# Kernel optimization log

Measured on AMD Instinct MI355X. Metric: run time of the kernel, lower is better.

Reference implementation:

```python
import jax, jax.numpy as jnp
import numpy as np

# irreps_in = irreps_out = 256x0e + 128x1o + 64x2e
MULS = [256, 128, 64]      # multiplicities per irrep
IRDIMS = [1, 3, 5]          # 2l+1 for l=0,1,2
N = 200000                  # number of atoms / nodes
DIM = sum(m * d for m, d in zip(MULS, IRDIMS))          # 960
WNUM = sum(m * m for m in MULS)                          # 86016
BNUM = MULS[0]                                           # bias only on scalar (0e) outputs


def setup_inputs() -> dict:
    key = jax.random.key(0)
    k1, k2, k3 = jax.random.split(key, 3)
    x = jax.random.normal(k1, (N, DIM), dtype=jnp.float32)
    w = jax.random.normal(k2, (WNUM,), dtype=jnp.float32)
    b = jax.random.normal(k3, (BNUM,), dtype=jnp.float32) * 0.1
    return {"x": x, "w": w, "b": b}


def reference(x, w, b):
    # Faithful to _codegen_linear with f_in=f_out=None, shared_weights=True:
    # per-irrep block einsum 'uw,zui->zwi' scaled by 1/sqrt(mul_in), plus bias on 0e block.
    n = x.shape[0]
    outs = []
    xoff = 0
    woff = 0
    for mul, d in zip(MULS, IRDIMS):
        blk = x[:, xoff:xoff + mul * d].reshape(n, mul, d)          # (N, u, i)
        W = w[woff:woff + mul * mul].reshape(mul, mul)              # (u, w)
        pw = mul ** -0.5                                            # path_weight (element norm)
        o = pw * jnp.einsum('uw,nui->nwi', W, blk)                  # (N, w, i)
        o = o.reshape(n, mul * d)
        if d == 1:  # scalar irrep: bias path, path_weight = 1
            o = o + b.reshape(1, mul)
        outs.append(o)
        xoff += mul * d
        woff += mul * mul
    return jnp.concatenate(outs, axis=-1)  # (N, 960)
```

## Files before the change

### kernel.cpp

```cpp
#include <hip/hip_runtime.h>


typedef short frag8 __attribute__((ext_vector_type(8)));
typedef float f32x4 __attribute__((ext_vector_type(4)));
typedef unsigned int u32;
typedef u32 u32x4 __attribute__((ext_vector_type(4)));

#define ST0 1040
#define ST1 1552
#define ST2 1296

static __device__ __forceinline__ short f2bf(float f) {
    union { float f; unsigned u; } v; v.f = f;
    unsigned r = (v.u + 0x7FFFu + ((v.u >> 16) & 1u)) >> 16;
    return (short)r;
}

static __device__ __forceinline__ u32 cvtpk(float lo, float hi) {
    u32 r;
    asm("v_cvt_pk_bf16_f32 %0, %1, %2" : "=v"(r) : "v"(lo), "v"(hi));
    return r;
}

static __device__ __forceinline__ frag8 asfrag(u32x4 u) {
    union { u32x4 u; frag8 f; } t; t.u = u; return t.f;
}

#define MFMA(a, b, c) __builtin_amdgcn_mfma_f32_16x16x32_bf16((a), (b), (c), 0, 0, 0)

__global__ __launch_bounds__(256) void prep_kernel(const float* __restrict__ w,
                                                   short* __restrict__ wf) {
    int e = blockIdx.x * 256 + threadIdx.x;
    int f = e >> 9;
    int r = e & 511;
    int l = r >> 3, j = r & 7;
    int l15 = l & 15, lg = l >> 4;
    int kk = 4 * lg + (j & 3) + 16 * (j >> 2);
    int u, wc, woff, mul; float scale;
    if (f < 128) {
        int nt = f >> 3, s = f & 7;
        u = 32 * s + kk; wc = nt * 16 + l15; woff = 0;     mul = 256; scale = 0.0625f;
    } else if (f < 160) {
        int g = f - 128, nt = g >> 2, s = g & 3;
        u = 32 * s + kk; wc = nt * 16 + l15; woff = 65536; mul = 128; scale = 0.088388347648318447f;
    } else {
        int g = f - 160, nt = g >> 1, s = g & 1;
        u = 32 * s + kk; wc = nt * 16 + l15; woff = 81920; mul = 64;  scale = 0.125f;
    }
    wf[e] = f2bf(scale * w[woff + u * mul + wc]);
}

static __device__ __forceinline__ void gload_lds16(const void* g, void* l) {
    __builtin_amdgcn_global_load_lds(
        (const __attribute__((address_space(1))) unsigned int*)g,
        (__attribute__((address_space(3))) unsigned int*)l, 16, 0, 0);
}

__global__ __launch_bounds__(256) void lin_t32(const float* __restrict__ x,
                                               const short* __restrict__ wf,
                                               const float* __restrict__ bias,
                                               float* __restrict__ out) {
    __shared__ __align__(16) char smem[32 * ST1];
    const int tid = threadIdx.x, lane = tid & 63, wv = tid >> 6;
    const int l15 = lane & 15, lg = lane >> 4;
    const int fam = blockIdx.y;
    const long rowbase = (long)blockIdx.x * 32;
    const char* __restrict__ xb = (const char*)x + rowbase * 3840;
    char* __restrict__ ob = (char*)out + rowbase * 3840;
    const frag8* __restrict__ wfr = (const frag8*)wf;

    if (fam == 0) {
        f32x4 bv[4];
        #pragma unroll
        for (int q = 0; q < 4; ++q)
            bv[q] = *(const f32x4*)(bias + (4 * wv + q) * 16 + 4 * lg);
        #pragma unroll
        for (int r8 = 0; r8 < 8; ++r8) {
            int r = 8 * wv + r8;
            gload_lds16(xb + (long)r * 3840 + (long)lane * 16, smem + r * ST0);
        }
        __syncthreads();

        const char* sbA = smem + l15 * ST0;
        frag8 a0[8];
        #pragma unroll
        for (int s = 0; s < 8; ++s) {
            const f32x4 v0 = *(const f32x4*)(sbA + (8 * s + lg) * 16);
            const f32x4 v1 = *(const f32x4*)(sbA + (8 * s + 4 + lg) * 16);
            u32x4 t = { cvtpk(v0[0], v0[1]), cvtpk(v0[2], v0[3]),
                        cvtpk(v1[0], v1[1]), cvtpk(v1[2], v1[3]) };
            a0[s] = asfrag(t);
        }
        __syncthreads();

        #pragma unroll
        for (int q = 0; q < 4; ++q) {
            const int nt = 4 * wv + q;
            f32x4 acc = {0.f, 0.f, 0.f, 0.f};
            #pragma unroll
            for (int s = 0; s < 8; ++s)
                acc = MFMA(wfr[(nt * 8 + s) * 64 + lane], a0[s], acc);
            const int g0 = nt * 4 + lg;
            *(f32x4*)(smem + l15 * ST0 + g0 * 16) = acc + bv[q];
        }
        const char* sbB = smem + (16 + l15) * ST0;
        frag8 a0b[8];
        #pragma unroll
        for (int s = 0; s < 8; ++s) {
            const f32x4 v0 = *(const f32x4*)(sbB + (8 * s + lg) * 16);
            const f32x4 v1 = *(const f32x4*)(sbB + (8 * s + 4 + lg) * 16);
            u32x4 t = { cvtpk(v0[0], v0[1]), cvtpk(v0[2], v0[3]),
                        cvtpk(v1[0], v1[1]), cvtpk(v1[2], v1[3]) };
            a0b[s] = asfrag(t);
        }
        __syncthreads();

        #pragma unroll
        for (int q = 0; q < 4; ++q) {
            const int nt = 4 * wv + q;
            f32x4 acc = {0.f, 0.f, 0.f, 0.f};
            #pragma unroll
            for (int s = 0; s < 8; ++s)
                acc = MFMA(wfr[(nt * 8 + s) * 64 + lane], a0b[s], acc);
            const int g0 = nt * 4 + lg;
            *(f32x4*)(smem + (16 + l15) * ST0 + g0 * 16) = acc + bv[q];
        }
        __syncthreads();

        #pragma unroll
        for (int j = 0; j < 8; ++j) {
            int c = j * 256 + tid, r = c >> 6, g = c & 63;
            f32x4 v = *(const f32x4*)(smem + r * ST0 + g * 16);
            *(f32x4*)(ob + (long)r * 3840 + g * 16) = v;
        }
    } else if (fam == 1) {
        frag8 w1[8];
        #pragma unroll
        for (int q = 0; q < 2; ++q)
            #pragma unroll
            for (int s = 0; s < 4; ++s)
                w1[q * 4 + s] = wfr[(128 + (2 * wv + q) * 4 + s) * 64 + lane];

        #pragma unroll
        for (int r8 = 0; r8 < 8; ++r8) {
            int r = 8 * wv + r8;
            gload_lds16(xb + (long)r * 3840 + 1024 + (long)lane * 16, smem + r * ST1);
            if (lane < 32)
                gload_lds16(xb + (long)r * 3840 + 2048 + (long)lane * 16,
                            smem + r * ST1 + 1024);
        }
        __syncthreads();

        {
            const char* sb = smem + l15 * ST1;
            u32x4 a1u[12];
            #pragma unroll
            for (int s = 0; s < 4; ++s) {
                #pragma unroll
                for (int h = 0; h < 2; ++h) {
                    const int cb = 24 * s + 12 * h + 3 * lg;
                    const f32x4 q0 = *(const f32x4*)(sb + (cb    ) * 16);
                    const f32x4 q1 = *(const f32x4*)(sb + (cb + 1) * 16);
                    const f32x4 q2 = *(const f32x4*)(sb + (cb + 2) * 16);
                    a1u[0 + s][2 * h]     = cvtpk(q0[0], q0[3]);
                    a1u[0 + s][2 * h + 1] = cvtpk(q1[2], q2[1]);
                    a1u[4 + s][2 * h]     = cvtpk(q0[1], q1[0]);
                    a1u[4 + s][2 * h + 1] = cvtpk(q1[3], q2[2]);
                    a1u[8 + s][2 * h]     = cvtpk(q0[2], q1[1]);
                    a1u[8 + s][2 * h + 1] = cvtpk(q2[0], q2[3]);
                }
            }
            __syncthreads();
            #pragma unroll
            for (int q = 0; q < 2; ++q) {
                const int nt = 2 * wv + q;
                f32x4 c0 = {0.f,0.f,0.f,0.f}, c1 = {0.f,0.f,0.f,0.f}, c2 = {0.f,0.f,0.f,0.f};
                #pragma unroll
                for (int s = 0; s < 4; ++s) {
                    frag8 bw = w1[q * 4 + s];
                    c0 = MFMA(bw, asfrag(a1u[0 + s]), c0);
                    c1 = MFMA(bw, asfrag(a1u[4 + s]), c1);
                    c2 = MFMA(bw, asfrag(a1u[8 + s]), c2);
                }
                const int g0 = 3 * (nt * 4 + lg);
                char* wb = smem + l15 * ST1;
                *(f32x4*)(wb + (g0    ) * 16) = (f32x4){c0[0], c1[0], c2[0], c0[1]};
                *(f32x4*)(wb + (g0 + 1) * 16) = (f32x4){c1[1], c2[1], c0[2], c1[2]};
                *(f32x4*)(wb + (g0 + 2) * 16) = (f32x4){c2[2], c0[3], c1[3], c2[3]};
            }
        }
        {
            const char* sb = smem + (16 + l15) * ST1;
            u32x4 a1u[12];
            #pragma unroll
            for (int s = 0; s < 4; ++s) {
                #pragma unroll
                for (int h = 0; h < 2; ++h) {
                    const int cb = 24 * s + 12 * h + 3 * lg;
                    const f32x4 q0 = *(const f32x4*)(sb + (cb    ) * 16);
                    const f32x4 q1 = *(const f32x4*)(sb + (cb + 1) * 16);
                    const f32x4 q2 = *(const f32x4*)(sb + (cb + 2) * 16);
                    a1u[0 + s][2 * h]     = cvtpk(q0[0], q0[3]);
                    a1u[0 + s][2 * h + 1] = cvtpk(q1[2], q2[1]);
                    a1u[4 + s][2 * h]     = cvtpk(q0[1], q1[0]);
                    a1u[4 + s][2 * h + 1] = cvtpk(q1[3], q2[2]);
                    a1u[8 + s][2 * h]     = cvtpk(q0[2], q1[1]);
                    a1u[8 + s][2 * h + 1] = cvtpk(q2[0], q2[3]);
                }
            }
            __syncthreads();
            #pragma unroll
            for (int q = 0; q < 2; ++q) {
                const int nt = 2 * wv + q;
                f32x4 c0 = {0.f,0.f,0.f,0.f}, c1 = {0.f,0.f,0.f,0.f}, c2 = {0.f,0.f,0.f,0.f};
                #pragma unroll
                for (int s = 0; s < 4; ++s) {
                    frag8 bw = w1[q * 4 + s];
                    c0 = MFMA(bw, asfrag(a1u[0 + s]), c0);
                    c1 = MFMA(bw, asfrag(a1u[4 + s]), c1);
                    c2 = MFMA(bw, asfrag(a1u[8 + s]), c2);
                }
                const int g0 = 3 * (nt * 4 + lg);
                char* wb = smem + (16 + l15) * ST1;
                *(f32x4*)(wb + (g0    ) * 16) = (f32x4){c0[0], c1[0], c2[0], c0[1]};
                *(f32x4*)(wb + (g0 + 1) * 16) = (f32x4){c1[1], c2[1], c0[2], c1[2]};
                *(f32x4*)(wb + (g0 + 2) * 16) = (f32x4){c2[2], c0[3], c1[3], c2[3]};
            }
        }
        __syncthreads();
        #pragma unroll
        for (int j = 0; j < 12; ++j) {
            int c = j * 256 + tid, r = c / 96, g = c - r * 96;
            f32x4 v = *(const f32x4*)(smem + r * ST1 + g * 16);
            *(f32x4*)(ob + (long)r * 3840 + 1024 + g * 16) = v;
        }
    } else {
        frag8 w2[2];
        #pragma unroll
        for (int s = 0; s < 2; ++s)
            w2[s] = wfr[(160 + wv * 2 + s) * 64 + lane];

        #pragma unroll
        for (int r8 = 0; r8 < 8; ++r8) {
            int r = 8 * wv + r8;
            gload_lds16(xb + (long)r * 3840 + 2560 + (long)lane * 16, smem + r * ST2);
            if (lane < 16)
                gload_lds16(xb + (long)r * 3840 + 3584 + (long)lane * 16,
                            smem + r * ST2 + 1024);
        }
        __syncthreads();

        #pragma unroll
        for (int half = 0; half < 2; ++half) {
            const int rbase = 16 * half;
            const char* sb = smem + (rbase + l15) * ST2;
            u32x4 a2u[10];
            #pragma unroll
            for (int s = 0; s < 2; ++s) {
                #pragma unroll
                for (int h = 0; h < 2; ++h) {
                    const int cb = 40 * s + 20 * h + 5 * lg;
                    const f32x4 q0 = *(const f32x4*)(sb + (cb    ) * 16);
                    const f32x4 q1 = *(const f32x4*)(sb + (cb + 1) * 16);
                    const f32x4 q2 = *(const f32x4*)(sb + (cb + 2) * 16);
                    const f32x4 q3 = *(const f32x4*)(sb + (cb + 3) * 16);
                    const f32x4 q4 = *(const f32x4*)(sb + (cb + 4) * 16);
                    a2u[0 + s][2 * h]     = cvtpk(q0[0], q1[1]);
                    a2u[0 + s][2 * h + 1] = cvtpk(q2[2], q3[3]);
                    a2u[2 + s][2 * h]     = cvtpk(q0[1], q1[2]);
                    a2u[2 + s][2 * h + 1] = cvtpk(q2[3], q4[0]);
                    a2u[4 + s][2 * h]     = cvtpk(q0[2], q1[3]);
                    a2u[4 + s][2 * h + 1] = cvtpk(q3[0], q4[1]);
                    a2u[6 + s][2 * h]     = cvtpk(q0[3], q2[0]);
                    a2u[6 + s][2 * h + 1] = cvtpk(q3[1], q4[2]);
                    a2u[8 + s][2 * h]     = cvtpk(q1[0], q2[1]);
                    a2u[8 + s][2 * h + 1] = cvtpk(q3[2], q4[3]);
                }
            }
            __syncthreads();
            {
                f32x4 c0 = {0.f,0.f,0.f,0.f}, c1 = {0.f,0.f,0.f,0.f}, c2 = {0.f,0.f,0.f,0.f},
                      c3 = {0.f,0.f,0.f,0.f}, c4 = {0.f,0.f,0.f,0.f};
                #pragma unroll
                for (int s = 0; s < 2; ++s) {
                    frag8 bw = w2[s];
                    c0 = MFMA(bw, asfrag(a2u[0 + s]), c0);
                    c1 = MFMA(bw, asfrag(a2u[2 + s]), c1);
                    c2 = MFMA(bw, asfrag(a2u[4 + s]), c2);
                    c3 = MFMA(bw, asfrag(a2u[6 + s]), c3);
                    c4 = MFMA(bw, asfrag(a2u[8 + s]), c4);
                }
                const int g0 = 5 * (wv * 4 + lg);
                char* wb = smem + (rbase + l15) * ST2;
                *(f32x4*)(wb + (g0    ) * 16) = (f32x4){c0[0], c1[0], c2[0], c3[0]};
                *(f32x4*)(wb + (g0 + 1) * 16) = (f32x4){c4[0], c0[1], c1[1], c2[1]};
                *(f32x4*)(wb + (g0 + 2) * 16) = (f32x4){c3[1], c4[1], c0[2], c1[2]};
                *(f32x4*)(wb + (g0 + 3) * 16) = (f32x4){c2[2], c3[2], c4[2], c0[3]};
                *(f32x4*)(wb + (g0 + 4) * 16) = (f32x4){c1[3], c2[3], c3[3], c4[3]};
            }
        }
        __syncthreads();
        #pragma unroll
        for (int j = 0; j < 10; ++j) {
            int c = j * 256 + tid, r = c / 80, g = c - r * 80;
            f32x4 v = *(const f32x4*)(smem + r * ST2 + g * 16);
            *(f32x4*)(ob + (long)r * 3840 + 2560 + g * 16) = v;
        }
    }
}

extern "C" void kernel_launch(void* const* d_in, const int* in_sizes, int n_in,
                              void* d_out, int out_size, void* d_ws, size_t ws_size,
                              hipStream_t stream) {
    const float* x = (const float*)d_in[0];
    const float* w = (const float*)d_in[1];
    const float* b = (const float*)d_in[2];
    float* out = (float*)d_out;
    short* wf  = (short*)d_ws;

    hipLaunchKernelGGL(prep_kernel, dim3(336), dim3(256), 0, stream, w, wf);
    hipLaunchKernelGGL(lin_t32, dim3(6250, 3), dim3(256), 0, stream,
                       x, wf, b, out);
}
```

Measured before the change: 324.4 us.

## Split fused per-irrep kernel into three specialized launches and merge half-tile phases

Replaces the single kernel, which branched on blockIdx.y to pick the irrep family, with three separate kernels. Each kernel sizes its shared memory to its own family, so the l=0 and l=2 kernels can fit more blocks per CU. Within each kernel, both 16-row halves are converted to bf16 before a single barrier, which removes intermediate syncthreads and lets their MFMAs interleave. The cost is more register pressure from holding both halves' fragments, plus two extra launches that run back to back instead of concurrently.

```diff
diff --git a/kernel.cpp b/kernel.cpp
--- a/kernel.cpp
+++ b/kernel.cpp
@@ -56,256 +56,241 @@
         (__attribute__((address_space(3))) unsigned int*)l, 16, 0, 0);
 }
 
-__global__ __launch_bounds__(256) void lin_t32(const float* __restrict__ x,
-                                               const short* __restrict__ wf,
-                                               const float* __restrict__ bias,
-                                               float* __restrict__ out) {
-    __shared__ __align__(16) char smem[32 * ST1];
+__global__ __launch_bounds__(256) void lin_a0(const float* __restrict__ x,
+                                              const short* __restrict__ wf,
+                                              const float* __restrict__ bias,
+                                              float* __restrict__ out) {
+    __shared__ __align__(16) char smem[32 * ST0];
     const int tid = threadIdx.x, lane = tid & 63, wv = tid >> 6;
     const int l15 = lane & 15, lg = lane >> 4;
-    const int fam = blockIdx.y;
     const long rowbase = (long)blockIdx.x * 32;
     const char* __restrict__ xb = (const char*)x + rowbase * 3840;
     char* __restrict__ ob = (char*)out + rowbase * 3840;
     const frag8* __restrict__ wfr = (const frag8*)wf;
 
-    if (fam == 0) {
-        f32x4 bv[4];
-        #pragma unroll
-        for (int q = 0; q < 4; ++q)
-            bv[q] = *(const f32x4*)(bias + (4 * wv + q) * 16 + 4 * lg);
-        #pragma unroll
-        for (int r8 = 0; r8 < 8; ++r8) {
-            int r = 8 * wv + r8;
-            gload_lds16(xb + (long)r * 3840 + (long)lane * 16, smem + r * ST0);
-        }
-        __syncthreads();
-
-        const char* sbA = smem + l15 * ST0;
-        frag8 a0[8];
+    f32x4 bv[4];
+    #pragma unroll
+    for (int q = 0; q < 4; ++q)
+        bv[q] = *(const f32x4*)(bias + (4 * wv + q) * 16 + 4 * lg);
+
+    #pragma unroll
+    for (int r8 = 0; r8 < 8; ++r8) {
+        int r = 8 * wv + r8;
+        gload_lds16(xb + (long)r * 3840 + (long)lane * 16, smem + r * ST0);
+    }
+    __syncthreads();
+
+    const char* sbA = smem + l15 * ST0;
+    const char* sbB = smem + (16 + l15) * ST0;
+    frag8 a0[8], a0b[8];
+    #pragma unroll
+    for (int s = 0; s < 8; ++s) {
+        const f32x4 v0 = *(const f32x4*)(sbA + (8 * s + lg) * 16);
+        const f32x4 v1 = *(const f32x4*)(sbA + (8 * s + 4 + lg) * 16);
+        u32x4 t = { cvtpk(v0[0], v0[1]), cvtpk(v0[2], v0[3]),
+                    cvtpk(v1[0], v1[1]), cvtpk(v1[2], v1[3]) };
+        a0[s] = asfrag(t);
+        const f32x4 w0 = *(const f32x4*)(sbB + (8 * s + lg) * 16);
+        const f32x4 w1v = *(const f32x4*)(sbB + (8 * s + 4 + lg) * 16);
+        u32x4 t2 = { cvtpk(w0[0], w0[1]), cvtpk(w0[2], w0[3]),
+                     cvtpk(w1v[0], w1v[1]), cvtpk(w1v[2], w1v[3]) };
+        a0b[s] = asfrag(t2);
+    }
+    __syncthreads();
+
+    #pragma unroll
+    for (int q = 0; q < 4; ++q) {
+        const int nt = 4 * wv + q;
+        f32x4 accA = {0.f, 0.f, 0.f, 0.f};
+        f32x4 accB = {0.f, 0.f, 0.f, 0.f};
         #pragma unroll
         for (int s = 0; s < 8; ++s) {
-            const f32x4 v0 = *(const f32x4*)(sbA + (8 * s + lg) * 16);
-            const f32x4 v1 = *(const f32x4*)(sbA + (8 * s + 4 + lg) * 16);
-            u32x4 t = { cvtpk(v0[0], v0[1]), cvtpk(v0[2], v0[3]),
-                        cvtpk(v1[0], v1[1]), cvtpk(v1[2], v1[3]) };
-            a0[s] = asfrag(t);
-        }
-        __syncthreads();
-
-        #pragma unroll
-        for (int q = 0; q < 4; ++q) {
-            const int nt = 4 * wv + q;
-            f32x4 acc = {0.f, 0.f, 0.f, 0.f};
+            frag8 bw = wfr[(nt * 8 + s) * 64 + lane];
+            accA = MFMA(bw, a0[s], accA);
+            accB = MFMA(bw, a0b[s], accB);
+        }
+        const int g0 = nt * 4 + lg;
+        *(f32x4*)(smem + l15 * ST0 + g0 * 16)        = accA + bv[q];
+        *(f32x4*)(smem + (16 + l15) * ST0 + g0 * 16) = accB + bv[q];
+    }
+    __syncthreads();
+
+    #pragma unroll
+    for (int j = 0; j < 8; ++j) {
+        int c = j * 256 + tid, r = c >> 6, g = c & 63;
+        f32x4 v = *(const f32x4*)(smem + r * ST0 + g * 16);
+        *(f32x4*)(ob + (long)r * 3840 + g * 16) = v;
+    }
+}
+
+__global__ __launch_bounds__(256) void lin_a1(const float* __restrict__ x,
+                                              const short* __restrict__ wf,
+                                              float* __restrict__ out) {
+    __shared__ __align__(16) char smem[32 * ST1];
+    const int tid = threadIdx.x, lane = tid & 63, wv = tid >> 6;
+    const int l15 = lane & 15, lg = lane >> 4;
+    const long rowbase = (long)blockIdx.x * 32;
+    const char* __restrict__ xb = (const char*)x + rowbase * 3840;
+    char* __restrict__ ob = (char*)out + rowbase * 3840;
+    const frag8* __restrict__ wfr = (const frag8*)wf;
+
+    frag8 w1[8];
+    #pragma unroll
+    for (int q = 0; q < 2; ++q)
+        #pragma unroll
+        for (int s = 0; s < 4; ++s)
+            w1[q * 4 + s] = wfr[(128 + (2 * wv + q) * 4 + s) * 64 + lane];
+
+    #pragma unroll
+    for (int r8 = 0; r8 < 8; ++r8) {
+        int r = 8 * wv + r8;
+        gload_lds16(xb + (long)r * 3840 + 1024 + (long)lane * 16, smem + r * ST1);
+        if (lane < 32)
+            gload_lds16(xb + (long)r * 3840 + 2048 + (long)lane * 16,
+                        smem + r * ST1 + 1024);
+    }
+    __syncthreads();
+
+    u32x4 aA[12], aB[12];
+    #pragma unroll
+    for (int half = 0; half < 2; ++half) {
+        const char* sb = smem + (16 * half + l15) * ST1;
+        u32x4* a1u = half ? aB : aA;
+        #pragma unroll
+        for (int s = 0; s < 4; ++s) {
             #pragma unroll
-            for (int s = 0; s < 8; ++s)
-                acc = MFMA(wfr[(nt * 8 + s) * 64 + lane], a0[s], acc);
-            const int g0 = nt * 4 + lg;
-            *(f32x4*)(smem + l15 * ST0 + g0 * 16) = acc + bv[q];
-        }
-        const char* sbB = smem + (16 + l15) * ST0;
-        frag8 a0b[8];
-        #pragma unroll
-        for (int s = 0; s < 8; ++s) {
-            const f32x4 v0 = *(const f32x4*)(sbB + (8 * s + lg) * 16);
-            const f32x4 v1 = *(const f32x4*)(sbB + (8 * s + 4 + lg) * 16);
-            u32x4 t = { cvtpk(v0[0], v0[1]), cvtpk(v0[2], v0[3]),
-                        cvtpk(v1[0], v1[1]), cvtpk(v1[2], v1[3]) };
-            a0b[s] = asfrag(t);
-        }
-        __syncthreads();
-
-        #pragma unroll
-        for (int q = 0; q < 4; ++q) {
-            const int nt = 4 * wv + q;
-            f32x4 acc = {0.f, 0.f, 0.f, 0.f};
-            #pragma unroll
-            for (int s = 0; s < 8; ++s)
-                acc = MFMA(wfr[(nt * 8 + s) * 64 + lane], a0b[s], acc);
-            const int g0 = nt * 4 + lg;
-            *(f32x4*)(smem + (16 + l15) * ST0 + g0 * 16) = acc + bv[q];
-        }
-        __syncthreads();
-
-        #pragma unroll
-        for (int j = 0; j < 8; ++j) {
-            int c = j * 256 + tid, r = c >> 6, g = c & 63;
-            f32x4 v = *(const f32x4*)(smem + r * ST0 + g * 16);
-            *(f32x4*)(ob + (long)r * 3840 + g * 16) = v;
-        }
-    } else if (fam == 1) {
-        frag8 w1[8];
-        #pragma unroll
-        for (int q = 0; q < 2; ++q)
-            #pragma unroll
-            for (int s = 0; s < 4; ++s)
-                w1[q * 4 + s] = wfr[(128 + (2 * wv + q) * 4 + s) * 64 + lane];
-
-        #pragma unroll
-        for (int r8 = 0; r8 < 8; ++r8) {
-            int r = 8 * wv + r8;
-            gload_lds16(xb + (long)r * 3840 + 1024 + (long)lane * 16, smem + r * ST1);
-            if (lane < 32)
-                gload_lds16(xb + (long)r * 3840 + 2048 + (long)lane * 16,
-                            smem + r * ST1 + 1024);
-        }
-        __syncthreads();
-
-        {
-            const char* sb = smem + l15 * ST1;
-            u32x4 a1u[12];
+            for (int h = 0; h < 2; ++h) {
+                const int cb = 24 * s + 12 * h + 3 * lg;
+                const f32x4 q0 = *(const f32x4*)(sb + (cb    ) * 16);
+                const f32x4 q1 = *(const f32x4*)(sb + (cb + 1) * 16);
+                const f32x4 q2 = *(const f32x4*)(sb + (cb + 2) * 16);
+                a1u[0 + s][2 * h]     = cvtpk(q0[0], q0[3]);
+                a1u[0 + s][2 * h + 1] = cvtpk(q1[2], q2[1]);
+                a1u[4 + s][2 * h]     = cvtpk(q0[1], q1[0]);
+                a1u[4 + s][2 * h + 1] = cvtpk(q1[3], q2[2]);
+                a1u[8 + s][2 * h]     = cvtpk(q0[2], q1[1]);
+                a1u[8 + s][2 * h + 1] = cvtpk(q2[0], q2[3]);
+            }
+        }
+    }
+    __syncthreads();
+
+    #pragma unroll
+    for (int half = 0; half < 2; ++half) {
+        const u32x4* a1u = half ? aB : aA;
+        char* wb = smem + (16 * half + l15) * ST1;
+        #pragma unroll
+        for (int q = 0; q < 2; ++q) {
+            const int nt = 2 * wv + q;
+            f32x4 c0 = {0.f,0.f,0.f,0.f}, c1 = {0.f,0.f,0.f,0.f}, c2 = {0.f,0.f,0.f,0.f};
             #pragma unroll
             for (int s = 0; s < 4; ++s) {
-                #pragma unroll
-                for (int h = 0; h < 2; ++h) {
-                    const int cb = 24 * s + 12 * h + 3 * lg;
-                    const f32x4 q0 = *(const f32x4*)(sb + (cb    ) * 16);
-                    const f32x4 q1 = *(const f32x4*)(sb + (cb + 1) * 16);
-                    const f32x4 q2 = *(const f32x4*)(sb + (cb + 2) * 16);
-                    a1u[0 + s][2 * h]     = cvtpk(q0[0], q0[3]);
-                    a1u[0 + s][2 * h + 1] = cvtpk(q1[2], q2[1]);
-                    a1u[4 + s][2 * h]     = cvtpk(q0[1], q1[0]);
-                    a1u[4 + s][2 * h + 1] = cvtpk(q1[3], q2[2]);
-                    a1u[8 + s][2 * h]     = cvtpk(q0[2], q1[1]);
-                    a1u[8 + s][2 * h + 1] = cvtpk(q2[0], q2[3]);
-                }
+                frag8 bw = w1[q * 4 + s];
+                c0 = MFMA(bw, asfrag(a1u[0 + s]), c0);
+                c1 = MFMA(bw, asfrag(a1u[4 + s]), c1);
+                c2 = MFMA(bw, asfrag(a1u[8 + s]), c2);
             }
-            __syncthreads();
+            const int g0 = 3 * (nt * 4 + lg);
+            *(f32x4*)(wb + (g0    ) * 16) = (f32x4){c0[0], c1[0], c2[0], c0[1]};
+            *(f32x4*)(wb + (g0 + 1) * 16) = (f32x4){c1[1], c2[1], c0[2], c1[2]};
+            *(f32x4*)(wb + (g0 + 2) * 16) = (f32x4){c2[2], c0[3], c1[3], c2[3]};
+        }
+    }
+    __syncthreads();
+
+    #pragma unroll
+    for (int j = 0; j < 12; ++j) {
+        int c = j * 256 + tid, r = c / 96, g = c - r * 96;
+        f32x4 v = *(const f32x4*)(smem + r * ST1 + g * 16);
+        *(f32x4*)(ob + (long)r * 3840 + 1024 + g * 16) = v;
+    }
+}
+
+__global__ __launch_bounds__(256) void lin_a2(const float* __restrict__ x,
+                                              const short* __restrict__ wf,
+                                              float* __restrict__ out) {
+    __shared__ __align__(16) char smem[32 * ST2];
+    const int tid = threadIdx.x, lane = tid & 63, wv = tid >> 6;
+    const int l15 = lane & 15, lg = lane >> 4;
+    const long rowbase = (long)blockIdx.x * 32;
+    const char* __restrict__ xb = (const char*)x + rowbase * 3840;
+    char* __restrict__ ob = (char*)out + rowbase * 3840;
+    const frag8* __restrict__ wfr = (const frag8*)wf;
+
+    frag8 w2[2];
+    #pragma unroll
+    for (int s = 0; s < 2; ++s)
+        w2[s] = wfr[(160 + wv * 2 + s) * 64 + lane];
+
+    #pragma unroll
+    for (int r8 = 0; r8 < 8; ++r8) {
+        int r = 8 * wv + r8;
+        gload_lds16(xb + (long)r * 3840 + 2560 + (long)lane * 16, smem + r * ST2);
+        if (lane < 16)
+            gload_lds16(xb + (long)r * 3840 + 3584 + (long)lane * 16,
+                        smem + r * ST2 + 1024);
+    }
+    __syncthreads();
+
+    u32x4 aA[10], aB[10];
+    #pragma unroll
+    for (int half = 0; half < 2; ++half) {
+        const char* sb = smem + (16 * half + l15) * ST2;
+        u32x4* a2u = half ? aB : aA;
+        #pragma unroll
+        for (int s = 0; s < 2; ++s) {
             #pragma unroll
-            for (int q = 0; q < 2; ++q) {
-                const int nt = 2 * wv + q;
-                f32x4 c0 = {0.f,0.f,0.f,0.f}, c1 = {0.f,0.f,0.f,0.f}, c2 = {0.f,0.f,0.f,0.f};
-                #pragma unroll
-                for (int s = 0; s < 4; ++s) {
-                    frag8 bw = w1[q * 4 + s];
-                    c0 = MFMA(bw, asfrag(a1u[0 + s]), c0);
-                    c1 = MFMA(bw, asfrag(a1u[4 + s]), c1);
-                    c2 = MFMA(bw, asfrag(a1u[8 + s]), c2);
-                }
-                const int g0 = 3 * (nt * 4 + lg);
-                char* wb = smem + l15 * ST1;
-                *(f32x4*)(wb + (g0    ) * 16) = (f32x4){c0[0], c1[0], c2[0], c0[1]};
-                *(f32x4*)(wb + (g0 + 1) * 16) = (f32x4){c1[1], c2[1], c0[2], c1[2]};
-                *(f32x4*)(wb + (g0 + 2) * 16) = (f32x4){c2[2], c0[3], c1[3], c2[3]};
+            for (int h = 0; h < 2; ++h) {
+                const int cb = 40 * s + 20 * h + 5 * lg;
+                const f32x4 q0 = *(const f32x4*)(sb + (cb    ) * 16);
+                const f32x4 q1 = *(const f32x4*)(sb + (cb + 1) * 16);
+                const f32x4 q2 = *(const f32x4*)(sb + (cb + 2) * 16);
+                const f32x4 q3 = *(const f32x4*)(sb + (cb + 3) * 16);
+                const f32x4 q4 = *(const f32x4*)(sb + (cb + 4) * 16);
+                a2u[0 + s][2 * h]     = cvtpk(q0[0], q1[1]);
+                a2u[0 + s][2 * h + 1] = cvtpk(q2[2], q3[3]);
+                a2u[2 + s][2 * h]     = cvtpk(q0[1], q1[2]);
+                a2u[2 + s][2 * h + 1] = cvtpk(q2[3], q4[0]);
+                a2u[4 + s][2 * h]     = cvtpk(q0[2], q1[3]);
+                a2u[4 + s][2 * h + 1] = cvtpk(q3[0], q4[1]);
+                a2u[6 + s][2 * h]     = cvtpk(q0[3], q2[0]);
+                a2u[6 + s][2 * h + 1] = cvtpk(q3[1], q4[2]);
+                a2u[8 + s][2 * h]     = cvtpk(q1[0], q2[1]);
+                a2u[8 + s][2 * h + 1] = cvtpk(q3[2], q4[3]);
             }
         }
-        {
-            const char* sb = smem + (16 + l15) * ST1;
-            u32x4 a1u[12];
-            #pragma unroll
-            for (int s = 0; s < 4; ++s) {
-                #pragma unroll
-                for (int h = 0; h < 2; ++h) {
-                    const int cb = 24 * s + 12 * h + 3 * lg;
-                    const f32x4 q0 = *(const f32x4*)(sb + (cb    ) * 16);
-                    const f32x4 q1 = *(const f32x4*)(sb + (cb + 1) * 16);
-                    const f32x4 q2 = *(const f32x4*)(sb + (cb + 2) * 16);
-                    a1u[0 + s][2 * h]     = cvtpk(q0[0], q0[3]);
-                    a1u[0 + s][2 * h + 1] = cvtpk(q1[2], q2[1]);
-                    a1u[4 + s][2 * h]     = cvtpk(q0[1], q1[0]);
-                    a1u[4 + s][2 * h + 1] = cvtpk(q1[3], q2[2]);
-                    a1u[8 + s][2 * h]     = cvtpk(q0[2], q1[1]);
-                    a1u[8 + s][2 * h + 1] = cvtpk(q2[0], q2[3]);
-                }
-            }
-            __syncthreads();
-            #pragma unroll
-            for (int q = 0; q < 2; ++q) {
-                const int nt = 2 * wv + q;
-                f32x4 c0 = {0.f,0.f,0.f,0.f}, c1 = {0.f,0.f,0.f,0.f}, c2 = {0.f,0.f,0.f,0.f};
-                #pragma unroll
-                for (int s = 0; s < 4; ++s) {
-                    frag8 bw = w1[q * 4 + s];
-                    c0 = MFMA(bw, asfrag(a1u[0 + s]), c0);
-                    c1 = MFMA(bw, asfrag(a1u[4 + s]), c1);
-                    c2 = MFMA(bw, asfrag(a1u[8 + s]), c2);
-                }
-                const int g0 = 3 * (nt * 4 + lg);
-                char* wb = smem + (16 + l15) * ST1;
-                *(f32x4*)(wb + (g0    ) * 16) = (f32x4){c0[0], c1[0], c2[0], c0[1]};
-                *(f32x4*)(wb + (g0 + 1) * 16) = (f32x4){c1[1], c2[1], c0[2], c1[2]};
-                *(f32x4*)(wb + (g0 + 2) * 16) = (f32x4){c2[2], c0[3], c1[3], c2[3]};
-            }
-        }
-        __syncthreads();
-        #pragma unroll
-        for (int j = 0; j < 12; ++j) {
-            int c = j * 256 + tid, r = c / 96, g = c - r * 96;
-            f32x4 v = *(const f32x4*)(smem + r * ST1 + g * 16);
-            *(f32x4*)(ob + (long)r * 3840 + 1024 + g * 16) = v;
-        }
-    } else {
-        frag8 w2[2];
-        #pragma unroll
-        for (int s = 0; s < 2; ++s)
-            w2[s] = wfr[(160 + wv * 2 + s) * 64 + lane];
-
-        #pragma unroll
-        for (int r8 = 0; r8 < 8; ++r8) {
-            int r = 8 * wv + r8;
-            gload_lds16(xb + (long)r * 3840 + 2560 + (long)lane * 16, smem + r * ST2);
-            if (lane < 16)
-                gload_lds16(xb + (long)r * 3840 + 3584 + (long)lane * 16,
-                            smem + r * ST2 + 1024);
-        }
-        __syncthreads();
-
-        #pragma unroll
-        for (int half = 0; half < 2; ++half) {
-            const int rbase = 16 * half;
-            const char* sb = smem + (rbase + l15) * ST2;
-            u32x4 a2u[10];
-            #pragma unroll
-            for (int s = 0; s < 2; ++s) {
-                #pragma unroll
-                for (int h = 0; h < 2; ++h) {
-                    const int cb = 40 * s + 20 * h + 5 * lg;
-                    const f32x4 q0 = *(const f32x4*)(sb + (cb    ) * 16);
-                    const f32x4 q1 = *(const f32x4*)(sb + (cb + 1) * 16);
-                    const f32x4 q2 = *(const f32x4*)(sb + (cb + 2) * 16);
-                    const f32x4 q3 = *(const f32x4*)(sb + (cb + 3) * 16);
-                    const f32x4 q4 = *(const f32x4*)(sb + (cb + 4) * 16);
-                    a2u[0 + s][2 * h]     = cvtpk(q0[0], q1[1]);
-                    a2u[0 + s][2 * h + 1] = cvtpk(q2[2], q3[3]);
-                    a2u[2 + s][2 * h]     = cvtpk(q0[1], q1[2]);
-                    a2u[2 + s][2 * h + 1] = cvtpk(q2[3], q4[0]);
-                    a2u[4 + s][2 * h]     = cvtpk(q0[2], q1[3]);
-                    a2u[4 + s][2 * h + 1] = cvtpk(q3[0], q4[1]);
-                    a2u[6 + s][2 * h]     = cvtpk(q0[3], q2[0]);
-                    a2u[6 + s][2 * h + 1] = cvtpk(q3[1], q4[2]);
-                    a2u[8 + s][2 * h]     = cvtpk(q1[0], q2[1]);
-                    a2u[8 + s][2 * h + 1] = cvtpk(q3[2], q4[3]);
-                }
-            }
-            __syncthreads();
-            {
-                f32x4 c0 = {0.f,0.f,0.f,0.f}, c1 = {0.f,0.f,0.f,0.f}, c2 = {0.f,0.f,0.f,0.f},
-                      c3 = {0.f,0.f,0.f,0.f}, c4 = {0.f,0.f,0.f,0.f};
-                #pragma unroll
-                for (int s = 0; s < 2; ++s) {
-                    frag8 bw = w2[s];
-                    c0 = MFMA(bw, asfrag(a2u[0 + s]), c0);
-                    c1 = MFMA(bw, asfrag(a2u[2 + s]), c1);
-                    c2 = MFMA(bw, asfrag(a2u[4 + s]), c2);
-                    c3 = MFMA(bw, asfrag(a2u[6 + s]), c3);
-                    c4 = MFMA(bw, asfrag(a2u[8 + s]), c4);
-                }
-                const int g0 = 5 * (wv * 4 + lg);
-                char* wb = smem + (rbase + l15) * ST2;
-                *(f32x4*)(wb + (g0    ) * 16) = (f32x4){c0[0], c1[0], c2[0], c3[0]};
-                *(f32x4*)(wb + (g0 + 1) * 16) = (f32x4){c4[0], c0[1], c1[1], c2[1]};
-                *(f32x4*)(wb + (g0 + 2) * 16) = (f32x4){c3[1], c4[1], c0[2], c1[2]};
-                *(f32x4*)(wb + (g0 + 3) * 16) = (f32x4){c2[2], c3[2], c4[2], c0[3]};
-                *(f32x4*)(wb + (g0 + 4) * 16) = (f32x4){c1[3], c2[3], c3[3], c4[3]};
-            }
-        }
-        __syncthreads();
-        #pragma unroll
-        for (int j = 0; j < 10; ++j) {
-            int c = j * 256 + tid, r = c / 80, g = c - r * 80;
-            f32x4 v = *(const f32x4*)(smem + r * ST2 + g * 16);
-            *(f32x4*)(ob + (long)r * 3840 + 2560 + g * 16) = v;
-        }
+    }
+    __syncthreads();
+
+    #pragma unroll
+    for (int half = 0; half < 2; ++half) {
+        const u32x4* a2u = half ? aB : aA;
+        char* wb = smem + (16 * half + l15) * ST2;
+        f32x4 c0 = {0.f,0.f,0.f,0.f}, c1 = {0.f,0.f,0.f,0.f}, c2 = {0.f,0.f,0.f,0.f},
+              c3 = {0.f,0.f,0.f,0.f}, c4 = {0.f,0.f,0.f,0.f};
+        #pragma unroll
+        for (int s = 0; s < 2; ++s) {
+            frag8 bw = w2[s];
+            c0 = MFMA(bw, asfrag(a2u[0 + s]), c0);
+            c1 = MFMA(bw, asfrag(a2u[2 + s]), c1);
+            c2 = MFMA(bw, asfrag(a2u[4 + s]), c2);
+            c3 = MFMA(bw, asfrag(a2u[6 + s]), c3);
+            c4 = MFMA(bw, asfrag(a2u[8 + s]), c4);
+        }
+        const int g0 = 5 * (wv * 4 + lg);
+        *(f32x4*)(wb + (g0    ) * 16) = (f32x4){c0[0], c1[0], c2[0], c3[0]};
+        *(f32x4*)(wb + (g0 + 1) * 16) = (f32x4){c4[0], c0[1], c1[1], c2[1]};
+        *(f32x4*)(wb + (g0 + 2) * 16) = (f32x4){c3[1], c4[1], c0[2], c1[2]};
+        *(f32x4*)(wb + (g0 + 3) * 16) = (f32x4){c2[2], c3[2], c4[2], c0[3]};
+        *(f32x4*)(wb + (g0 + 4) * 16) = (f32x4){c1[3], c2[3], c3[3], c4[3]};
+    }
+    __syncthreads();
+
+    #pragma unroll
+    for (int j = 0; j < 10; ++j) {
+        int c = j * 256 + tid, r = c / 80, g = c - r * 80;
+        f32x4 v = *(const f32x4*)(smem + r * ST2 + g * 16);
+        *(f32x4*)(ob + (long)r * 3840 + 2560 + g * 16) = v;
     }
 }
 
@@ -319,6 +304,7 @@
     short* wf  = (short*)d_ws;
 
     hipLaunchKernelGGL(prep_kernel, dim3(336), dim3(256), 0, stream, w, wf);
-    hipLaunchKernelGGL(lin_t32, dim3(6250, 3), dim3(256), 0, stream,
-                       x, wf, b, out);
-}
+    hipLaunchKernelGGL(lin_a1, dim3(6250), dim3(256), 0, stream, x, wf, out);
+    hipLaunchKernelGGL(lin_a0, dim3(6250), dim3(256), 0, stream, x, wf, b, out);
+    hipLaunchKernelGGL(lin_a2, dim3(6250), dim3(256), 0, stream, x, wf, out);
+}
```

After: 348.3 us. 1.07x slower.
